# Kernel tuning notes

Hardware: AMD Instinct MI355X
Metric: run time of the kernel (lower is better)

## Reference

```python
import jax, jax.numpy as jnp
import numpy as np

D = 2048
NH = 16
DH = D // NH          # 128
DC = D // 4           # 512  (KV latent)
DCQ = D // 2          # 1024 (Q latent)
B = 1
L = 2048
MAX_LEN = 4096


def precompute_rope(dh, max_len):
    inv_freq = 1.0 / (10000.0 ** (jnp.arange(0, dh, 2, dtype=jnp.float32) / dh))
    t = jnp.arange(max_len, dtype=jnp.float32)
    freqs = jnp.outer(t, inv_freq)                 # [max_len, dh/2]
    emb = jnp.concatenate([freqs, freqs], axis=-1) # [max_len, dh]
    return jnp.cos(emb), jnp.sin(emb)


def apply_rope(t, cos, sin):
    # t: [B, H, L, dh]; cos/sin: [L, dh]
    x1, x2 = jnp.split(t, 2, axis=-1)
    rot = jnp.concatenate([-x2, x1], axis=-1)
    return t * cos + rot * sin


def setup_inputs() -> dict:
    key = jax.random.key(0)
    ks = jax.random.split(key, 9)
    s = 0.02
    return {
        "x": jax.random.normal(ks[0], (B, L, D), dtype=jnp.float32),
        "W_DKV": jax.random.normal(ks[1], (D, DC), dtype=jnp.float32) * s,
        "W_UK": jax.random.normal(ks[2], (DC, NH * DH), dtype=jnp.float32) * s,
        "W_UV": jax.random.normal(ks[3], (DC, NH * DH), dtype=jnp.float32) * s,
        "W_DQ": jax.random.normal(ks[4], (D, DCQ), dtype=jnp.float32) * s,
        "W_UQ": jax.random.normal(ks[5], (DCQ, 2 * NH * DH), dtype=jnp.float32) * s,
        "W_lam": jax.random.normal(ks[6], (D, NH), dtype=jnp.float32) * s,
        "b_lam": jnp.zeros((NH,), dtype=jnp.float32),
        "W_out": jax.random.normal(ks[7], (D, D), dtype=jnp.float32) * s,
    }


def reference(x, W_DKV, W_UK, W_UV, W_DQ, W_UQ, W_lam, b_lam, W_out):
    Bx, Lx, Dx = x.shape
    cos, sin = precompute_rope(DH, MAX_LEN)
    cos, sin = cos[:Lx], sin[:Lx]

    # MLA KV compression: single K/V shared by the paired query heads
    c_kv = x @ W_DKV                                            # [B, L, dc]
    k = (c_kv @ W_UK).reshape(Bx, Lx, NH, DH).transpose(0, 2, 1, 3)   # [B, nh, L, dh]
    v = (c_kv @ W_UV).reshape(Bx, Lx, NH, DH).transpose(0, 2, 1, 3)   # [B, nh, L, dh]

    # Low-rank Q, doubled heads for differential attention
    c_q = x @ W_DQ                                              # [B, L, dcq]
    q = (c_q @ W_UQ).reshape(Bx, Lx, 2 * NH, DH).transpose(0, 2, 1, 3)  # [B, 2nh, L, dh]

    q = apply_rope(q, cos, sin)
    k = apply_rope(k, cos, sin)

    # Group paired heads (2i, 2i+1) share k/v head i -> avoid repeat_interleave
    qp = q.reshape(Bx, NH, 2, Lx, DH)                           # [B, nh, 2, L, dh]
    scale = 1.0 / jnp.sqrt(jnp.asarray(DH, dtype=x.dtype))
    scores = jnp.einsum('bhpqd,bhkd->bhpqk', qp, k) * scale     # [B, nh, 2, L, L]
    causal = jnp.tril(jnp.ones((Lx, Lx), dtype=bool))
    scores = jnp.where(causal, scores, jnp.asarray(-jnp.inf, dtype=scores.dtype))
    probs = jax.nn.softmax(scores, axis=-1)
    attn = jnp.einsum('bhpqk,bhkd->bhpqd', probs, v)            # [B, nh, 2, L, dh]
    attn1, attn2 = attn[:, :, 0], attn[:, :, 1]                 # [B, nh, L, dh]

    # Token-specific sigmoid lambda per head
    lam = jax.nn.sigmoid(x @ W_lam + b_lam)                     # [B, L, nh]
    lam = lam.transpose(0, 2, 1)[..., None]                     # [B, nh, L, 1]

    out = (attn1 - lam * attn2).transpose(0, 2, 1, 3).reshape(Bx, Lx, Dx)
    return out @ W_out
```

## Files before the change

### kernel.cpp

```cpp
#include <hip/hip_runtime.h>
#include <cstdint>
#include <cstddef>

typedef __bf16 bf16x8 __attribute__((ext_vector_type(8)));
typedef __bf16 bf16x4 __attribute__((ext_vector_type(4)));
typedef float f32x4 __attribute__((ext_vector_type(4)));


template <int BM, bool BF16OUT>
__device__ __forceinline__ void gemm_body(const __bf16* __restrict__ A,
                                          const __bf16* __restrict__ Bt,
                                          void* __restrict__ Cv,
                                          int N, int K, int bm, int bn,
                                          __bf16* As, __bf16* Bs) {
  const int tid = threadIdx.x;
  const int w = tid >> 6;
  const int lane = tid & 63;
  const int quad = lane >> 4;
  const int l16 = lane & 15;
  constexpr int WM = (BM == 128) ? 64 : 32;
  constexpr int MI = WM / 16;
  const int wm = (w & 1) * WM;
  const int wn = (w >> 1) * 64;
  const int srow = lane >> 2;
  const int sseg = (lane & 3) * 8;

  auto stage = [&](int k0, int buf) {
#pragma unroll
    for (int g = 0; g < BM / 64; ++g) {
      const int grp = w + g * 4;
      const __bf16* ga = A + (size_t)(bm + grp * 16 + srow) * K + k0 + sseg;
      __builtin_amdgcn_global_load_lds(
          (const __attribute__((address_space(1))) void*)ga,
          (__attribute__((address_space(3))) void*)&As[buf * (BM * 32) + grp * 512],
          16, 0, 0);
    }
#pragma unroll
    for (int g = 0; g < 2; ++g) {
      const int grp = w + g * 4;
      const __bf16* gb = Bt + (size_t)(bn + grp * 16 + srow) * K + k0 + sseg;
      __builtin_amdgcn_global_load_lds(
          (const __attribute__((address_space(1))) void*)gb,
          (__attribute__((address_space(3))) void*)&Bs[buf * 4096 + grp * 512],
          16, 0, 0);
    }
  };

  f32x4 acc[MI][4];
#pragma unroll
  for (int i = 0; i < MI; ++i)
#pragma unroll
    for (int j = 0; j < 4; ++j) acc[i][j] = (f32x4){0.f, 0.f, 0.f, 0.f};

  asm volatile("s_waitcnt vmcnt(0)" ::: "memory");
  stage(0, 0);

  const int NIT = K >> 5;
  for (int it = 0; it < NIT; ++it) {
    const int cur = it & 1;
    if (it + 1 < NIT) {
      stage((it + 1) << 5, cur ^ 1);
      if constexpr (BM == 64)
        asm volatile("s_waitcnt vmcnt(3)" ::: "memory");
      else
        asm volatile("s_waitcnt vmcnt(4)" ::: "memory");
    } else {
      asm volatile("s_waitcnt vmcnt(0)" ::: "memory");
    }
    __builtin_amdgcn_s_barrier();
    asm volatile("" ::: "memory");
    const __bf16* Ab = &As[cur * (BM * 32)];
    const __bf16* Bb = &Bs[cur * 4096];
    bf16x8 af[MI], bfr[4];
#pragma unroll
    for (int i = 0; i < MI; ++i)
      af[i] = *(const bf16x8*)&Ab[(wm + i * 16 + l16) * 32 + quad * 8];
#pragma unroll
    for (int j = 0; j < 4; ++j)
      bfr[j] = *(const bf16x8*)&Bb[(wn + j * 16 + l16) * 32 + quad * 8];
#pragma unroll
    for (int i = 0; i < MI; ++i)
#pragma unroll
      for (int j = 0; j < 4; ++j)
        acc[i][j] = __builtin_amdgcn_mfma_f32_16x16x32_bf16(af[i], bfr[j],
                                                            acc[i][j], 0, 0, 0);
    asm volatile("s_waitcnt lgkmcnt(0)" ::: "memory");
    __builtin_amdgcn_s_barrier();
    asm volatile("" ::: "memory");
  }
#pragma unroll
  for (int i = 0; i < MI; ++i)
#pragma unroll
    for (int j = 0; j < 4; ++j)
#pragma unroll
      for (int r = 0; r < 4; ++r) {
        const int row = bm + wm + i * 16 + quad * 4 + r;
        const int col = bn + wn + j * 16 + l16;
        if constexpr (BF16OUT)
          ((__bf16*)Cv)[(size_t)row * N + col] = (__bf16)acc[i][j][r];
        else
          ((float*)Cv)[(size_t)row * N + col] = acc[i][j][r];
      }
}

template <int BM, bool BF16OUT>
__global__ __launch_bounds__(256) void gemm_mfma(const __bf16* __restrict__ A,
                                                 const __bf16* __restrict__ Bt,
                                                 void* __restrict__ Cv,
                                                 int M, int N, int K) {
  __shared__ __bf16 As[2 * BM * 32];
  __shared__ __bf16 Bs[2 * 128 * 32];
  gemm_body<BM, BF16OUT>(A, Bt, Cv, N, K, blockIdx.y * BM, blockIdx.x * 128, As, Bs);
}

template <int BM>
__global__ __launch_bounds__(256) void gemm_fused3(
    const __bf16* A0, const __bf16* B0, __bf16* C0, int N0, int K0, int nx0,
    const __bf16* A1, const __bf16* B1, __bf16* C1, int N1, int K1, int nx1,
    const __bf16* A2, const __bf16* B2, __bf16* C2, int N2, int K2) {
  __shared__ __bf16 As[2 * BM * 32];
  __shared__ __bf16 Bs[2 * 128 * 32];
  const int bx = blockIdx.x;
  const __bf16 *A, *Bt;
  __bf16* C;
  int N, K, bxl;
  if (bx < nx0)            { A = A0; Bt = B0; C = C0; N = N0; K = K0; bxl = bx; }
  else if (bx < nx0 + nx1) { A = A1; Bt = B1; C = C1; N = N1; K = K1; bxl = bx - nx0; }
  else                     { A = A2; Bt = B2; C = C2; N = N2; K = K2; bxl = bx - nx0 - nx1; }
  gemm_body<BM, true>(A, Bt, (void*)C, N, K, blockIdx.y * BM, bxl * 128, As, Bs);
}

__global__ __launch_bounds__(256) void prep_all(
    const float* __restrict__ W_DKV, const float* __restrict__ W_DQ,
    const float* __restrict__ W_UK,  const float* __restrict__ W_UV,
    const float* __restrict__ W_UQ,  const float* __restrict__ W_out,
    const float* __restrict__ x,     const float* __restrict__ W_lam,
    __bf16* __restrict__ tDKV, __bf16* __restrict__ tDQ,
    __bf16* __restrict__ tUK,  __bf16* __restrict__ tUV,
    __bf16* __restrict__ tUQ,  __bf16* __restrict__ tOut,
    __bf16* __restrict__ x_bf, __bf16* __restrict__ WlT,
    float* __restrict__ cosT, float* __restrict__ sinT) {
  __shared__ float T[32][36];
  int t = blockIdx.x;
  const int tid = threadIdx.x;
  if (t < 13312) {
    const float* src; __bf16* dst; int K, N, kx, ny;
    if (t < 1024)      {            src = W_DKV; dst = tDKV; K = 2048; N = 512;  kx = t & 63; ny = t >> 6; }
    else if (t < 3072) { t -= 1024; src = W_DQ;  dst = tDQ;  K = 2048; N = 1024; kx = t & 63; ny = t >> 6; }
    else if (t < 4096) { t -= 3072; src = W_UK;  dst = tUK;  K = 512;  N = 2048; kx = t & 15; ny = t >> 4; }
    else if (t < 5120) { t -= 4096; src = W_UV;  dst = tUV;  K = 512;  N = 2048; kx = t & 15; ny = t >> 4; }
    else if (t < 9216) { t -= 5120; src = W_UQ;  dst = tUQ;  K = 1024; N = 4096; kx = t & 31; ny = t >> 5; }
    else               { t -= 9216; src = W_out; dst = tOut; K = 2048; N = 2048; kx = t & 63; ny = t >> 6; }
    const int k0 = kx * 32;
    const int n0 = ny * 32;
    const int r = tid >> 3;
    const int c = (tid & 7) * 4;
    *(float4*)&T[r][c] = *(const float4*)&src[(size_t)(k0 + r) * N + n0 + c];
    __syncthreads();
    bf16x4 o = {(__bf16)T[c + 0][r], (__bf16)T[c + 1][r],
                (__bf16)T[c + 2][r], (__bf16)T[c + 3][r]};
    *(bf16x4*)&dst[(size_t)(n0 + r) * K + k0 + c] = o;
    return;
  }
  t -= 13312;
  if (t < 4096) {
    const int i = t * 256 + tid;
    float4 v = *(const float4*)&x[(size_t)i * 4];
    bf16x4 o = {(__bf16)v.x, (__bf16)v.y, (__bf16)v.z, (__bf16)v.w};
    *(bf16x4*)&x_bf[(size_t)i * 4] = o;
    return;
  }
  t -= 4096;
  if (t < 1024) {
    const int l = t * 2 + (tid >> 7);
    const int d = tid & 127;
    const int j = d & 63;
    const float inv = exp2f(-(float)j * 0.2076205059304601f);
    const float ang = (float)l * inv;
    cosT[l * 128 + d] = cosf(ang);
    sinT[l * 128 + d] = sinf(ang);
    return;
  }
  t -= 1024;
  {
    const int i = t * 256 + tid;
    const int k = i >> 4, n = i & 15;
    WlT[(size_t)n * 2048 + k] = (__bf16)W_lam[i];
  }
}

__global__ __launch_bounds__(256) void ropek_transv(__bf16* __restrict__ k_bf,
                                                    const float* __restrict__ cosT,
                                                    const float* __restrict__ sinT,
                                                    const __bf16* __restrict__ v_bf,
                                                    __bf16* __restrict__ v_t) {
  __shared__ float row[2048];
  __shared__ __align__(16) __bf16 Ts[32][40];
  int t = blockIdx.x;
  const int tid = threadIdx.x;
  if (t < 2048) {
    __bf16* rp = k_bf + (size_t)t * 2048;
#pragma unroll
    for (int i = 0; i < 2; ++i) {
      const int e4 = (tid + 256 * i) * 4;
      bf16x4 v = *(const bf16x4*)&rp[e4];
#pragma unroll
      for (int k = 0; k < 4; ++k) row[e4 + k] = (float)v[k];
    }
    __syncthreads();
#pragma unroll
    for (int i = 0; i < 8; ++i) {
      const int e = tid + 256 * i;
      const int d = e & 127;
      const float c = cosT[t * 128 + d];
      const float s = sinT[t * 128 + d];
      const float tv = row[e];
      const int base = e & ~127;
      const float rot = (d < 64) ? -row[base + d + 64] : row[base + d - 64];
      rp[e] = (__bf16)(tv * c + rot * s);
    }
    return;
  }
  t -= 2048;
  const int l0 = (t & 63) * 32;
  const int d0 = (t >> 6) * 32;
  const int r = tid >> 3;
  const int c = (tid & 7) * 4;
  *(bf16x4*)&Ts[r][c] = *(const bf16x4*)&v_bf[(size_t)(l0 + r) * 2048 + d0 + c];
  __syncthreads();
  bf16x4 o = {Ts[c + 0][r], Ts[c + 1][r], Ts[c + 2][r], Ts[c + 3][r]};
  *(bf16x4*)&v_t[(size_t)(d0 + r) * 2048 + l0 + c] = o;
}

__global__ __launch_bounds__(256) void lam_mfma_kernel(const __bf16* __restrict__ x_bf,
                                                       const __bf16* __restrict__ WlT,
                                                       const float* __restrict__ b_lam,
                                                       float* __restrict__ lam) {
  const int tid = threadIdx.x;
  const int w = tid >> 6, lane = tid & 63, quad = lane >> 4, l16 = lane & 15;
  const int m0 = (blockIdx.x * 4 + w) * 16;
  const __bf16* xrow = x_bf + (size_t)(m0 + l16) * 2048 + quad * 8;
  const __bf16* wrow = WlT + (size_t)l16 * 2048 + quad * 8;
  f32x4 acc[4];
#pragma unroll
  for (int u = 0; u < 4; ++u) acc[u] = (f32x4){0.f, 0.f, 0.f, 0.f};
  for (int k0 = 0; k0 < 2048; k0 += 128) {
#pragma unroll
    for (int u = 0; u < 4; ++u) {
      bf16x8 a = *(const bf16x8*)&xrow[k0 + u * 32];
      bf16x8 b = *(const bf16x8*)&wrow[k0 + u * 32];
      acc[u] = __builtin_amdgcn_mfma_f32_16x16x32_bf16(a, b, acc[u], 0, 0, 0);
    }
  }
  const float bl = b_lam[l16];
#pragma unroll
  for (int r = 0; r < 4; ++r) {
    const float v = acc[0][r] + acc[1][r] + acc[2][r] + acc[3][r] + bl;
    lam[(size_t)(m0 + quad * 4 + r) * 16 + l16] = 1.0f / (1.0f + __expf(-v));
  }
}

__global__ __launch_bounds__(256, 2) void attn_kernel3(
    const __bf16* __restrict__ Qb, const __bf16* __restrict__ Kb,
    const __bf16* __restrict__ Vt, const float* __restrict__ cosT,
    const float* __restrict__ sinT, const float* __restrict__ lam,
    __bf16* __restrict__ y) {
  __shared__ __align__(16) char smem[81920];
  float (*Ex)[132] = (float(*)[132])smem;

  const int bx = blockIdx.x;
  const int hv = bx >> 8;
  const int ii = bx & 255;
  const int qt = hv ? (ii >> 4) : 31 - (ii >> 4);
  const int hk = ii & 15;
  const int q0 = qt * 64;
  const int tid = threadIdx.x;
  const int w = tid >> 6, lane = tid & 63, quad = lane >> 4, l16 = lane & 15;
  const int wrow = (w & 1) * 32;
  const int qoff = (2 * hk + (w >> 1)) * 128;
  const int kvoff = hk * 128;
  const float qscale = 0.08838834764831845f;
  char* Pw = smem + 65536 + w * (32 * 128);

  bf16x8 aq[2][4];
#pragma unroll
  for (int s = 0; s < 2; ++s) {
    const int l = q0 + wrow + s * 16 + l16;
    const size_t qbase = (size_t)l * 4096 + qoff + quad * 8;
    bf16x8 raw[4];
#pragma unroll
    for (int ks = 0; ks < 4; ++ks)
      raw[ks] = *(const bf16x8*)&Qb[qbase + ks * 32];
#pragma unroll
    for (int ks = 0; ks < 4; ++ks) {
      const float* cp = &cosT[l * 128 + ks * 32 + quad * 8];
      const float* sp = &sinT[l * 128 + ks * 32 + quad * 8];
#pragma unroll
      for (int j = 0; j < 8; ++j) {
        const float cv = cp[j];
        const float sv = sp[j];
        const float rot = (ks < 2) ? -(float)raw[ks + 2][j] : (float)raw[ks - 2][j];
        aq[s][ks][j] = (__bf16)(((float)raw[ks][j] * cv + rot * sv) * qscale);
      }
    }
  }

  auto stage = [&](int kt_, char* buf) {
    const int k0_ = kt_ * 64;
    __bf16* Ksb = (__bf16*)buf;
    __bf16* Vsb = (__bf16*)(buf + 16384);
#pragma unroll
    for (int d = 0; d < 4; ++d) {
      const int r0 = w * 16 + d * 4;
      const int row = r0 + (lane >> 4);
      const int ck = (lane & 15) ^ (row & 15);
      const __bf16* ga = Kb + (size_t)(k0_ + row) * 2048 + kvoff + ck * 8;
      __builtin_amdgcn_global_load_lds(
          (const __attribute__((address_space(1))) void*)ga,
          (__attribute__((address_space(3))) void*)&Ksb[r0 * 128], 16, 0, 0);
      const int r0v = w * 32 + d * 8;
      const int rowv = r0v + (lane >> 3);
      const int cv = (lane & 7) ^ (rowv & 7);
      const __bf16* gv = Vt + (size_t)(kvoff + rowv) * 2048 + k0_ + cv * 8;
      __builtin_amdgcn_global_load_lds(
          (const __attribute__((address_space(1))) void*)gv,
          (__attribute__((address_space(3))) void*)&Vsb[r0v * 64], 16, 0, 0);
    }
  };

  f32x4 o[2][8];
#pragma unroll
  for (int s = 0; s < 2; ++s)
#pragma unroll
    for (int i = 0; i < 8; ++i) o[s][i] = (f32x4){0.f, 0.f, 0.f, 0.f};
  float m[2] = {-1e30f, -1e30f}, lsum[2] = {0.f, 0.f};

  asm volatile("s_waitcnt vmcnt(0)" ::: "memory");
  stage(0, smem);

  for (int kt = 0; kt <= qt; ++kt) {
    const int cur = kt & 1;
    __bf16* Ks = (__bf16*)(smem + cur * 32768);
    __bf16* Vs = (__bf16*)(smem + cur * 32768 + 16384);
    const int k0 = kt * 64;
    if (kt < qt) {
      stage(kt + 1, smem + (cur ^ 1) * 32768);
      asm volatile("s_waitcnt vmcnt(8)" ::: "memory");
    } else {
      asm volatile("s_waitcnt vmcnt(0)" ::: "memory");
    }
    __builtin_amdgcn_s_barrier();
    asm volatile("" ::: "memory");
    f32x4 st[2][4];
#pragma unroll
    for (int s = 0; s < 2; ++s)
#pragma unroll
      for (int t = 0; t < 4; ++t) st[s][t] = (f32x4){0.f, 0.f, 0.f, 0.f};
    __builtin_amdgcn_s_setprio(1);
#pragma unroll
    for (int ks = 0; ks < 4; ++ks) {
#pragma unroll
      for (int t = 0; t < 4; ++t) {
        bf16x8 ak = *(bf16x8*)&Ks[(t * 16 + l16) * 128 + (((ks * 4 + quad) ^ l16) << 3)];
        st[0][t] = __builtin_amdgcn_mfma_f32_16x16x32_bf16(ak, aq[0][ks], st[0][t], 0, 0, 0);
        st[1][t] = __builtin_amdgcn_mfma_f32_16x16x32_bf16(ak, aq[1][ks], st[1][t], 0, 0, 0);
      }
    }
    __builtin_amdgcn_s_setprio(0);
    const bool masked = (kt == qt);
#pragma unroll
    for (int s = 0; s < 2; ++s) {
      const int q = q0 + wrow + s * 16 + l16;
      float rm = -1e30f;
      if (!masked) {
#pragma unroll
        for (int t = 0; t < 4; ++t)
#pragma unroll
          for (int r = 0; r < 4; ++r) rm = fmaxf(rm, st[s][t][r]);
      } else {
#pragma unroll
        for (int t = 0; t < 4; ++t)
#pragma unroll
          for (int r = 0; r < 4; ++r) {
            const int key = k0 + t * 16 + quad * 4 + r;
            if (key > q) st[s][t][r] = -1e30f;
            rm = fmaxf(rm, st[s][t][r]);
          }
      }
      rm = fmaxf(rm, __shfl_xor(rm, 16, 64));
      rm = fmaxf(rm, __shfl_xor(rm, 32, 64));
      const float mn = fmaxf(m[s], rm);
      const float alpha = __expf(m[s] - mn);
      float rs = 0.f;
#pragma unroll
      for (int t = 0; t < 4; ++t)
#pragma unroll
        for (int r = 0; r < 4; ++r) {
          st[s][t][r] = __expf(st[s][t][r] - mn);
          rs += st[s][t][r];
        }
      rs += __shfl_xor(rs, 16, 64);
      rs += __shfl_xor(rs, 32, 64);
      m[s] = mn;
      lsum[s] = lsum[s] * alpha + rs;
      const int prow = s * 16 + l16;
#pragma unroll
      for (int t = 0; t < 4; ++t) {
        bf16x4 pk = {(__bf16)st[s][t][0], (__bf16)st[s][t][1],
                     (__bf16)st[s][t][2], (__bf16)st[s][t][3]};
        const int wch = (t * 2 + (quad >> 1)) ^ (prow & 7);
        *(bf16x4*)(Pw + prow * 128 + wch * 16 + (quad & 1) * 8) = pk;
      }
#pragma unroll
      for (int r = 0; r < 4; ++r) {
        const float ar = __shfl(alpha, quad * 4 + r, 64);
#pragma unroll
        for (int nt = 0; nt < 8; ++nt) o[s][nt][r] *= ar;
      }
    }
    __builtin_amdgcn_s_setprio(1);
#pragma unroll
    for (int ks = 0; ks < 2; ++ks) {
      const int rch = ((ks * 4 + quad) ^ (l16 & 7)) << 4;
      bf16x8 pa0 = *(bf16x8*)(Pw + l16 * 128 + rch);
      bf16x8 pa1 = *(bf16x8*)(Pw + (16 + l16) * 128 + rch);
#pragma unroll
      for (int nt = 0; nt < 8; ++nt) {
        bf16x8 bv = *(bf16x8*)&Vs[(nt * 16 + l16) * 64 + (((ks * 4 + quad) ^ (l16 & 7)) << 3)];
        o[0][nt] = __builtin_amdgcn_mfma_f32_16x16x32_bf16(pa0, bv, o[0][nt], 0, 0, 0);
        o[1][nt] = __builtin_amdgcn_mfma_f32_16x16x32_bf16(pa1, bv, o[1][nt], 0, 0, 0);
      }
    }
    __builtin_amdgcn_s_setprio(0);
    asm volatile("s_waitcnt lgkmcnt(0)" ::: "memory");
    __builtin_amdgcn_s_barrier();
    asm volatile("" ::: "memory");
  }
  if (w >= 2) {
#pragma unroll
    for (int s = 0; s < 2; ++s) {
      const float linv = 1.0f / lsum[s];
#pragma unroll
      for (int r = 0; r < 4; ++r) {
        const float inv = __shfl(linv, quad * 4 + r, 64);
        const int rr = wrow + s * 16 + quad * 4 + r;
#pragma unroll
        for (int nt = 0; nt < 8; ++nt)
          Ex[rr][nt * 16 + l16] = o[s][nt][r] * inv;
      }
    }
  }
  __syncthreads();
  if (w < 2) {
#pragma unroll
    for (int s = 0; s < 2; ++s) {
      const float linv = 1.0f / lsum[s];
#pragma unroll
      for (int r = 0; r < 4; ++r) {
        const float inv = __shfl(linv, quad * 4 + r, 64);
        const int rr = wrow + s * 16 + quad * 4 + r;
        const int l = q0 + rr;
        const float lm = lam[l * 16 + hk];
        __bf16* dst = y + (size_t)l * 2048 + hk * 128;
#pragma unroll
        for (int nt = 0; nt < 8; ++nt) {
          const float v1 = o[s][nt][r] * inv;
          dst[nt * 16 + l16] = (__bf16)(v1 - lm * Ex[rr][nt * 16 + l16]);
        }
      }
    }
  }
}

extern "C" void kernel_launch(void* const* d_in, const int* in_sizes, int n_in,
                              void* d_out, int out_size, void* d_ws, size_t ws_size,
                              hipStream_t stream) {
  const float* x     = (const float*)d_in[0];
  const float* W_DKV = (const float*)d_in[1];
  const float* W_UK  = (const float*)d_in[2];
  const float* W_UV  = (const float*)d_in[3];
  const float* W_DQ  = (const float*)d_in[4];
  const float* W_UQ  = (const float*)d_in[5];
  const float* W_lam = (const float*)d_in[6];
  const float* b_lam = (const float*)d_in[7];
  const float* W_out = (const float*)d_in[8];
  float* out = (float*)d_out;

  char* ws = (char*)d_ws;
  #define MB(n) ((size_t)(n) << 20)
  __bf16* x_bf   = (__bf16*)(ws + MB(0));
  __bf16* Wt_DKV = (__bf16*)(ws + MB(8));
  __bf16* Wt_DQ  = (__bf16*)(ws + MB(10));
  __bf16* c_kv   = (__bf16*)(ws + MB(14));
  __bf16* c_q    = (__bf16*)(ws + MB(16));
  __bf16* Wt_UK  = (__bf16*)(ws + MB(20));
  __bf16* Wt_UV  = (__bf16*)(ws + MB(22));
  __bf16* Wt_UQ  = (__bf16*)(ws + MB(24));
  __bf16* k_bf   = (__bf16*)(ws + MB(32));
  __bf16* v_bf   = (__bf16*)(ws + MB(40));
  __bf16* y_bf   = (__bf16*)(ws + MB(40));
  __bf16* q_bf   = (__bf16*)(ws + MB(48));
  __bf16* v_t    = (__bf16*)(ws + MB(64));
  float*  lam    = (float*)(ws + MB(88));
  float*  cosT   = (float*)(ws + MB(89));
  float*  sinT   = (float*)(ws + MB(90));
  __bf16* WlT    = (__bf16*)(ws + MB(91));
  __bf16* Wt_out = (__bf16*)(ws + MB(92));

  prep_all<<<18560, 256, 0, stream>>>(W_DKV, W_DQ, W_UK, W_UV, W_UQ, W_out,
                                      x, W_lam,
                                      Wt_DKV, Wt_DQ, Wt_UK, Wt_UV, Wt_UQ, Wt_out,
                                      x_bf, WlT, cosT, sinT);
  gemm_fused3<64><<<dim3(12, 32), 256, 0, stream>>>(
      x_bf, Wt_DKV, c_kv, 512, 2048, 4,
      x_bf, Wt_DQ,  c_q, 1024, 2048, 8,
      x_bf, Wt_DQ,  c_q, 1024, 2048);
  lam_mfma_kernel<<<32, 256, 0, stream>>>(x_bf, WlT, b_lam, lam);
  gemm_fused3<128><<<dim3(64, 16), 256, 0, stream>>>(
      c_kv, Wt_UK, k_bf, 2048, 512, 16,
      c_kv, Wt_UV, v_bf, 2048, 512, 16,
      c_q,  Wt_UQ, q_bf, 4096, 1024);
  ropek_transv<<<6144, 256, 0, stream>>>(k_bf, cosT, sinT, v_bf, v_t);
  attn_kernel3<<<512, 256, 0, stream>>>(q_bf, k_bf, v_t, cosT, sinT, lam, y_bf);
  gemm_mfma<64, false><<<dim3(16, 32), 256, 0, stream>>>(y_bf, Wt_out, out, 2048, 2048, 2048);
}
```

Before: 324.0 us.

## Double attention wave count, add conditional rescale, and deepen GEMM K-stage

The attention kernel now runs 512 threads per block, so each wave handles 16 query rows instead of 32. This halves per-wave registers and spreads K/V staging across more waves. The online softmax skips rescaling the output accumulator when no row maximum changed. The GEMMs gain an NKS template that loads two 32-wide K slices per barrier, halving barrier count at the cost of doubled LDS. The larger attention block with 80KB of LDS risks lower occupancy, and the launch_bounds(512,2) may limit registers.

```diff
diff --git a/kernel.cpp b/kernel.cpp
--- a/kernel.cpp
+++ b/kernel.cpp
@@ -7,7 +7,15 @@
 typedef float f32x4 __attribute__((ext_vector_type(4)));
 
 
-template <int BM, bool BF16OUT>
+template <int N> __device__ __forceinline__ void waitcnt_vm() {
+  if constexpr (N == 3)      asm volatile("s_waitcnt vmcnt(3)" ::: "memory");
+  else if constexpr (N == 4) asm volatile("s_waitcnt vmcnt(4)" ::: "memory");
+  else if constexpr (N == 6) asm volatile("s_waitcnt vmcnt(6)" ::: "memory");
+  else if constexpr (N == 8) asm volatile("s_waitcnt vmcnt(8)" ::: "memory");
+  else                       asm volatile("s_waitcnt vmcnt(0)" ::: "memory");
+}
+
+template <int BM, int NKS, bool BF16OUT>
 __device__ __forceinline__ void gemm_body(const __bf16* __restrict__ A,
                                           const __bf16* __restrict__ Bt,
                                           void* __restrict__ Cv,
@@ -20,6 +28,7 @@
   const int l16 = lane & 15;
   constexpr int WM = (BM == 128) ? 64 : 32;
   constexpr int MI = WM / 16;
+  constexpr int NL = NKS * (BM / 64 + 2);
   const int wm = (w & 1) * WM;
   const int wn = (w >> 1) * 64;
   const int srow = lane >> 2;
@@ -27,22 +36,25 @@
 
   auto stage = [&](int k0, int buf) {
 #pragma unroll
-    for (int g = 0; g < BM / 64; ++g) {
-      const int grp = w + g * 4;
-      const __bf16* ga = A + (size_t)(bm + grp * 16 + srow) * K + k0 + sseg;
-      __builtin_amdgcn_global_load_lds(
-          (const __attribute__((address_space(1))) void*)ga,
-          (__attribute__((address_space(3))) void*)&As[buf * (BM * 32) + grp * 512],
-          16, 0, 0);
-    }
-#pragma unroll
-    for (int g = 0; g < 2; ++g) {
-      const int grp = w + g * 4;
-      const __bf16* gb = Bt + (size_t)(bn + grp * 16 + srow) * K + k0 + sseg;
-      __builtin_amdgcn_global_load_lds(
-          (const __attribute__((address_space(1))) void*)gb,
-          (__attribute__((address_space(3))) void*)&Bs[buf * 4096 + grp * 512],
-          16, 0, 0);
+    for (int ks = 0; ks < NKS; ++ks) {
+#pragma unroll
+      for (int g = 0; g < BM / 64; ++g) {
+        const int grp = w + g * 4;
+        const __bf16* ga = A + (size_t)(bm + grp * 16 + srow) * K + k0 + ks * 32 + sseg;
+        __builtin_amdgcn_global_load_lds(
+            (const __attribute__((address_space(1))) void*)ga,
+            (__attribute__((address_space(3))) void*)&As[(buf * NKS + ks) * (BM * 32) + grp * 512],
+            16, 0, 0);
+      }
+#pragma unroll
+      for (int g = 0; g < 2; ++g) {
+        const int grp = w + g * 4;
+        const __bf16* gb = Bt + (size_t)(bn + grp * 16 + srow) * K + k0 + ks * 32 + sseg;
+        __builtin_amdgcn_global_load_lds(
+            (const __attribute__((address_space(1))) void*)gb,
+            (__attribute__((address_space(3))) void*)&Bs[(buf * NKS + ks) * 4096 + grp * 512],
+            16, 0, 0);
+      }
     }
   };
 
@@ -55,35 +67,35 @@
   asm volatile("s_waitcnt vmcnt(0)" ::: "memory");
   stage(0, 0);
 
-  const int NIT = K >> 5;
+  const int NIT = K / (32 * NKS);
   for (int it = 0; it < NIT; ++it) {
     const int cur = it & 1;
     if (it + 1 < NIT) {
-      stage((it + 1) << 5, cur ^ 1);
-      if constexpr (BM == 64)
-        asm volatile("s_waitcnt vmcnt(3)" ::: "memory");
-      else
-        asm volatile("s_waitcnt vmcnt(4)" ::: "memory");
+      stage((it + 1) * 32 * NKS, cur ^ 1);
+      waitcnt_vm<NL>();
     } else {
-      asm volatile("s_waitcnt vmcnt(0)" ::: "memory");
+      waitcnt_vm<0>();
     }
     __builtin_amdgcn_s_barrier();
     asm volatile("" ::: "memory");
-    const __bf16* Ab = &As[cur * (BM * 32)];
-    const __bf16* Bb = &Bs[cur * 4096];
-    bf16x8 af[MI], bfr[4];
-#pragma unroll
-    for (int i = 0; i < MI; ++i)
-      af[i] = *(const bf16x8*)&Ab[(wm + i * 16 + l16) * 32 + quad * 8];
-#pragma unroll
-    for (int j = 0; j < 4; ++j)
-      bfr[j] = *(const bf16x8*)&Bb[(wn + j * 16 + l16) * 32 + quad * 8];
-#pragma unroll
-    for (int i = 0; i < MI; ++i)
+    const __bf16* Ab = &As[cur * NKS * (BM * 32)];
+    const __bf16* Bb = &Bs[cur * NKS * 4096];
+#pragma unroll
+    for (int ks = 0; ks < NKS; ++ks) {
+      bf16x8 af[MI], bfr[4];
+#pragma unroll
+      for (int i = 0; i < MI; ++i)
+        af[i] = *(const bf16x8*)&Ab[ks * (BM * 32) + (wm + i * 16 + l16) * 32 + quad * 8];
 #pragma unroll
       for (int j = 0; j < 4; ++j)
-        acc[i][j] = __builtin_amdgcn_mfma_f32_16x16x32_bf16(af[i], bfr[j],
-                                                            acc[i][j], 0, 0, 0);
+        bfr[j] = *(const bf16x8*)&Bb[ks * 4096 + (wn + j * 16 + l16) * 32 + quad * 8];
+#pragma unroll
+      for (int i = 0; i < MI; ++i)
+#pragma unroll
+        for (int j = 0; j < 4; ++j)
+          acc[i][j] = __builtin_amdgcn_mfma_f32_16x16x32_bf16(af[i], bfr[j],
+                                                              acc[i][j], 0, 0, 0);
+    }
     asm volatile("s_waitcnt lgkmcnt(0)" ::: "memory");
     __builtin_amdgcn_s_barrier();
     asm volatile("" ::: "memory");
@@ -103,23 +115,23 @@
       }
 }
 
-template <int BM, bool BF16OUT>
+template <int BM, int NKS, bool BF16OUT>
 __global__ __launch_bounds__(256) void gemm_mfma(const __bf16* __restrict__ A,
                                                  const __bf16* __restrict__ Bt,
                                                  void* __restrict__ Cv,
                                                  int M, int N, int K) {
-  __shared__ __bf16 As[2 * BM * 32];
-  __shared__ __bf16 Bs[2 * 128 * 32];
-  gemm_body<BM, BF16OUT>(A, Bt, Cv, N, K, blockIdx.y * BM, blockIdx.x * 128, As, Bs);
-}
-
-template <int BM>
+  __shared__ __bf16 As[2 * BM * 32 * NKS];
+  __shared__ __bf16 Bs[2 * 128 * 32 * NKS];
+  gemm_body<BM, NKS, BF16OUT>(A, Bt, Cv, N, K, blockIdx.y * BM, blockIdx.x * 128, As, Bs);
+}
+
+template <int BM, int NKS>
 __global__ __launch_bounds__(256) void gemm_fused3(
     const __bf16* A0, const __bf16* B0, __bf16* C0, int N0, int K0, int nx0,
     const __bf16* A1, const __bf16* B1, __bf16* C1, int N1, int K1, int nx1,
     const __bf16* A2, const __bf16* B2, __bf16* C2, int N2, int K2) {
-  __shared__ __bf16 As[2 * BM * 32];
-  __shared__ __bf16 Bs[2 * 128 * 32];
+  __shared__ __bf16 As[2 * BM * 32 * NKS];
+  __shared__ __bf16 Bs[2 * 128 * 32 * NKS];
   const int bx = blockIdx.x;
   const __bf16 *A, *Bt;
   __bf16* C;
@@ -127,7 +139,7 @@
   if (bx < nx0)            { A = A0; Bt = B0; C = C0; N = N0; K = K0; bxl = bx; }
   else if (bx < nx0 + nx1) { A = A1; Bt = B1; C = C1; N = N1; K = K1; bxl = bx - nx0; }
   else                     { A = A2; Bt = B2; C = C2; N = N2; K = K2; bxl = bx - nx0 - nx1; }
-  gemm_body<BM, true>(A, Bt, (void*)C, N, K, blockIdx.y * BM, bxl * 128, As, Bs);
+  gemm_body<BM, NKS, true>(A, Bt, (void*)C, N, K, blockIdx.y * BM, bxl * 128, As, Bs);
 }
 
 __global__ __launch_bounds__(256) void prep_all(
@@ -260,7 +272,7 @@
   }
 }
 
-__global__ __launch_bounds__(256, 2) void attn_kernel3(
+__global__ __launch_bounds__(512, 2) void attn_kernel3(
     const __bf16* __restrict__ Qb, const __bf16* __restrict__ Kb,
     const __bf16* __restrict__ Vt, const float* __restrict__ cosT,
     const float* __restrict__ sinT, const float* __restrict__ lam,
@@ -276,16 +288,15 @@
   const int q0 = qt * 64;
   const int tid = threadIdx.x;
   const int w = tid >> 6, lane = tid & 63, quad = lane >> 4, l16 = lane & 15;
-  const int wrow = (w & 1) * 32;
-  const int qoff = (2 * hk + (w >> 1)) * 128;
+  const int wrow = (w & 3) * 16;
+  const int qoff = (2 * hk + (w >> 2)) * 128;
   const int kvoff = hk * 128;
   const float qscale = 0.08838834764831845f;
-  char* Pw = smem + 65536 + w * (32 * 128);
-
-  bf16x8 aq[2][4];
-#pragma unroll
-  for (int s = 0; s < 2; ++s) {
-    const int l = q0 + wrow + s * 16 + l16;
+  char* Pw = smem + 65536 + w * 2048;
+
+  bf16x8 aq[4];
+  {
+    const int l = q0 + wrow + l16;
     const size_t qbase = (size_t)l * 4096 + qoff + quad * 8;
     bf16x8 raw[4];
 #pragma unroll
@@ -300,7 +311,7 @@
         const float cv = cp[j];
         const float sv = sp[j];
         const float rot = (ks < 2) ? -(float)raw[ks + 2][j] : (float)raw[ks - 2][j];
-        aq[s][ks][j] = (__bf16)(((float)raw[ks][j] * cv + rot * sv) * qscale);
+        aq[ks][j] = (__bf16)(((float)raw[ks][j] * cv + rot * sv) * qscale);
       }
     }
   }
@@ -310,15 +321,15 @@
     __bf16* Ksb = (__bf16*)buf;
     __bf16* Vsb = (__bf16*)(buf + 16384);
 #pragma unroll
-    for (int d = 0; d < 4; ++d) {
-      const int r0 = w * 16 + d * 4;
+    for (int d = 0; d < 2; ++d) {
+      const int r0 = w * 8 + d * 4;
       const int row = r0 + (lane >> 4);
       const int ck = (lane & 15) ^ (row & 15);
       const __bf16* ga = Kb + (size_t)(k0_ + row) * 2048 + kvoff + ck * 8;
       __builtin_amdgcn_global_load_lds(
           (const __attribute__((address_space(1))) void*)ga,
           (__attribute__((address_space(3))) void*)&Ksb[r0 * 128], 16, 0, 0);
-      const int r0v = w * 32 + d * 8;
+      const int r0v = w * 16 + d * 8;
       const int rowv = r0v + (lane >> 3);
       const int cv = (lane & 7) ^ (rowv & 7);
       const __bf16* gv = Vt + (size_t)(kvoff + rowv) * 2048 + k0_ + cv * 8;
@@ -328,12 +339,10 @@
     }
   };
 
-  f32x4 o[2][8];
-#pragma unroll
-  for (int s = 0; s < 2; ++s)
-#pragma unroll
-    for (int i = 0; i < 8; ++i) o[s][i] = (f32x4){0.f, 0.f, 0.f, 0.f};
-  float m[2] = {-1e30f, -1e30f}, lsum[2] = {0.f, 0.f};
+  f32x4 o[8];
+#pragma unroll
+  for (int i = 0; i < 8; ++i) o[i] = (f32x4){0.f, 0.f, 0.f, 0.f};
+  float m = -1e30f, lsum = 0.f;
 
   asm volatile("s_waitcnt vmcnt(0)" ::: "memory");
   stage(0, smem);
@@ -345,90 +354,87 @@
     const int k0 = kt * 64;
     if (kt < qt) {
       stage(kt + 1, smem + (cur ^ 1) * 32768);
-      asm volatile("s_waitcnt vmcnt(8)" ::: "memory");
+      asm volatile("s_waitcnt vmcnt(4)" ::: "memory");
     } else {
       asm volatile("s_waitcnt vmcnt(0)" ::: "memory");
     }
     __builtin_amdgcn_s_barrier();
     asm volatile("" ::: "memory");
-    f32x4 st[2][4];
-#pragma unroll
-    for (int s = 0; s < 2; ++s)
-#pragma unroll
-      for (int t = 0; t < 4; ++t) st[s][t] = (f32x4){0.f, 0.f, 0.f, 0.f};
+    f32x4 st[4];
+#pragma unroll
+    for (int t = 0; t < 4; ++t) st[t] = (f32x4){0.f, 0.f, 0.f, 0.f};
     __builtin_amdgcn_s_setprio(1);
 #pragma unroll
     for (int ks = 0; ks < 4; ++ks) {
 #pragma unroll
       for (int t = 0; t < 4; ++t) {
         bf16x8 ak = *(bf16x8*)&Ks[(t * 16 + l16) * 128 + (((ks * 4 + quad) ^ l16) << 3)];
-        st[0][t] = __builtin_amdgcn_mfma_f32_16x16x32_bf16(ak, aq[0][ks], st[0][t], 0, 0, 0);
-        st[1][t] = __builtin_amdgcn_mfma_f32_16x16x32_bf16(ak, aq[1][ks], st[1][t], 0, 0, 0);
+        st[t] = __builtin_amdgcn_mfma_f32_16x16x32_bf16(ak, aq[ks], st[t], 0, 0, 0);
       }
     }
     __builtin_amdgcn_s_setprio(0);
-    const bool masked = (kt == qt);
-#pragma unroll
-    for (int s = 0; s < 2; ++s) {
-      const int q = q0 + wrow + s * 16 + l16;
+    {
+      const int q = q0 + wrow + l16;
       float rm = -1e30f;
-      if (!masked) {
+      if (kt != qt) {
 #pragma unroll
         for (int t = 0; t < 4; ++t)
 #pragma unroll
-          for (int r = 0; r < 4; ++r) rm = fmaxf(rm, st[s][t][r]);
+          for (int r = 0; r < 4; ++r) rm = fmaxf(rm, st[t][r]);
       } else {
 #pragma unroll
         for (int t = 0; t < 4; ++t)
 #pragma unroll
           for (int r = 0; r < 4; ++r) {
             const int key = k0 + t * 16 + quad * 4 + r;
-            if (key > q) st[s][t][r] = -1e30f;
-            rm = fmaxf(rm, st[s][t][r]);
+            if (key > q) st[t][r] = -1e30f;
+            rm = fmaxf(rm, st[t][r]);
           }
       }
       rm = fmaxf(rm, __shfl_xor(rm, 16, 64));
       rm = fmaxf(rm, __shfl_xor(rm, 32, 64));
-      const float mn = fmaxf(m[s], rm);
-      const float alpha = __expf(m[s] - mn);
+      const float mn = fmaxf(m, rm);
       float rs = 0.f;
 #pragma unroll
       for (int t = 0; t < 4; ++t)
 #pragma unroll
         for (int r = 0; r < 4; ++r) {
-          st[s][t][r] = __expf(st[s][t][r] - mn);
-          rs += st[s][t][r];
+          st[t][r] = __expf(st[t][r] - mn);
+          rs += st[t][r];
         }
       rs += __shfl_xor(rs, 16, 64);
       rs += __shfl_xor(rs, 32, 64);
-      m[s] = mn;
-      lsum[s] = lsum[s] * alpha + rs;
-      const int prow = s * 16 + l16;
+      if (__any(rm > m)) {
+        const float alpha = __expf(m - mn);
+        lsum = lsum * alpha + rs;
+        m = mn;
+#pragma unroll
+        for (int r = 0; r < 4; ++r) {
+          const float ar = __shfl(alpha, quad * 4 + r, 64);
+#pragma unroll
+          for (int nt = 0; nt < 8; ++nt) o[nt][r] *= ar;
+        }
+      } else {
+        lsum += rs;
+      }
+      const int prow = l16;
 #pragma unroll
       for (int t = 0; t < 4; ++t) {
-        bf16x4 pk = {(__bf16)st[s][t][0], (__bf16)st[s][t][1],
-                     (__bf16)st[s][t][2], (__bf16)st[s][t][3]};
+        bf16x4 pk = {(__bf16)st[t][0], (__bf16)st[t][1],
+                     (__bf16)st[t][2], (__bf16)st[t][3]};
         const int wch = (t * 2 + (quad >> 1)) ^ (prow & 7);
         *(bf16x4*)(Pw + prow * 128 + wch * 16 + (quad & 1) * 8) = pk;
       }
-#pragma unroll
-      for (int r = 0; r < 4; ++r) {
-        const float ar = __shfl(alpha, quad * 4 + r, 64);
-#pragma unroll
-        for (int nt = 0; nt < 8; ++nt) o[s][nt][r] *= ar;
-      }
     }
     __builtin_amdgcn_s_setprio(1);
 #pragma unroll
     for (int ks = 0; ks < 2; ++ks) {
       const int rch = ((ks * 4 + quad) ^ (l16 & 7)) << 4;
-      bf16x8 pa0 = *(bf16x8*)(Pw + l16 * 128 + rch);
-      bf16x8 pa1 = *(bf16x8*)(Pw + (16 + l16) * 128 + rch);
+      bf16x8 pa = *(bf16x8*)(Pw + l16 * 128 + rch);
 #pragma unroll
       for (int nt = 0; nt < 8; ++nt) {
         bf16x8 bv = *(bf16x8*)&Vs[(nt * 16 + l16) * 64 + (((ks * 4 + quad) ^ (l16 & 7)) << 3)];
-        o[0][nt] = __builtin_amdgcn_mfma_f32_16x16x32_bf16(pa0, bv, o[0][nt], 0, 0, 0);
-        o[1][nt] = __builtin_amdgcn_mfma_f32_16x16x32_bf16(pa1, bv, o[1][nt], 0, 0, 0);
+        o[nt] = __builtin_amdgcn_mfma_f32_16x16x32_bf16(pa, bv, o[nt], 0, 0, 0);
       }
     }
     __builtin_amdgcn_s_setprio(0);
@@ -436,37 +442,30 @@
     __builtin_amdgcn_s_barrier();
     asm volatile("" ::: "memory");
   }
-  if (w >= 2) {
-#pragma unroll
-    for (int s = 0; s < 2; ++s) {
-      const float linv = 1.0f / lsum[s];
-#pragma unroll
-      for (int r = 0; r < 4; ++r) {
-        const float inv = __shfl(linv, quad * 4 + r, 64);
-        const int rr = wrow + s * 16 + quad * 4 + r;
-#pragma unroll
-        for (int nt = 0; nt < 8; ++nt)
-          Ex[rr][nt * 16 + l16] = o[s][nt][r] * inv;
-      }
+  const float linv = 1.0f / lsum;
+  if (w >= 4) {
+#pragma unroll
+    for (int r = 0; r < 4; ++r) {
+      const float inv = __shfl(linv, quad * 4 + r, 64);
+      const int rr = wrow + quad * 4 + r;
+#pragma unroll
+      for (int nt = 0; nt < 8; ++nt)
+        Ex[rr][nt * 16 + l16] = o[nt][r] * inv;
     }
   }
   __syncthreads();
-  if (w < 2) {
-#pragma unroll
-    for (int s = 0; s < 2; ++s) {
-      const float linv = 1.0f / lsum[s];
-#pragma unroll
-      for (int r = 0; r < 4; ++r) {
-        const float inv = __shfl(linv, quad * 4 + r, 64);
-        const int rr = wrow + s * 16 + quad * 4 + r;
-        const int l = q0 + rr;
-        const float lm = lam[l * 16 + hk];
-        __bf16* dst = y + (size_t)l * 2048 + hk * 128;
-#pragma unroll
-        for (int nt = 0; nt < 8; ++nt) {
-          const float v1 = o[s][nt][r] * inv;
-          dst[nt * 16 + l16] = (__bf16)(v1 - lm * Ex[rr][nt * 16 + l16]);
-        }
+  if (w < 4) {
+#pragma unroll
+    for (int r = 0; r < 4; ++r) {
+      const float inv = __shfl(linv, quad * 4 + r, 64);
+      const int rr = wrow + quad * 4 + r;
+      const int l = q0 + rr;
+      const float lm = lam[l * 16 + hk];
+      __bf16* dst = y + (size_t)l * 2048 + hk * 128;
+#pragma unroll
+      for (int nt = 0; nt < 8; ++nt) {
+        const float v1 = o[nt][r] * inv;
+        dst[nt * 16 + l16] = (__bf16)(v1 - lm * Ex[rr][nt * 16 + l16]);
       }
     }
   }
@@ -511,16 +510,16 @@
                                       x, W_lam,
                                       Wt_DKV, Wt_DQ, Wt_UK, Wt_UV, Wt_UQ, Wt_out,
                                       x_bf, WlT, cosT, sinT);
-  gemm_fused3<64><<<dim3(12, 32), 256, 0, stream>>>(
+  gemm_fused3<64, 2><<<dim3(12, 32), 256, 0, stream>>>(
       x_bf, Wt_DKV, c_kv, 512, 2048, 4,
       x_bf, Wt_DQ,  c_q, 1024, 2048, 8,
       x_bf, Wt_DQ,  c_q, 1024, 2048);
   lam_mfma_kernel<<<32, 256, 0, stream>>>(x_bf, WlT, b_lam, lam);
-  gemm_fused3<128><<<dim3(64, 16), 256, 0, stream>>>(
+  gemm_fused3<128, 1><<<dim3(64, 16), 256, 0, stream>>>(
       c_kv, Wt_UK, k_bf, 2048, 512, 16,
       c_kv, Wt_UV, v_bf, 2048, 512, 16,
       c_q,  Wt_UQ, q_bf, 4096, 1024);
   ropek_transv<<<6144, 256, 0, stream>>>(k_bf, cosT, sinT, v_bf, v_t);
-  attn_kernel3<<<512, 256, 0, stream>>>(q_bf, k_bf, v_t, cosT, sinT, lam, y_bf);
-  gemm_mfma<64, false><<<dim3(16, 32), 256, 0, stream>>>(y_bf, Wt_out, out, 2048, 2048, 2048);
-}
+  attn_kernel3<<<512, 512, 0, stream>>>(q_bf, k_bf, v_t, cosT, sinT, lam, y_bf);
+  gemm_mfma<64, 2, false><<<dim3(16, 32), 256, 0, stream>>>(y_bf, Wt_out, out, 2048, 2048, 2048);
+}
```

Result: faster. 306.1 us (-5.5%).
